# Optimization experiments

Hardware: AMD Instinct MI355X
Metric: run time of the kernel (lower is better)

The kernel has to match this reference:

```python
import jax, jax.numpy as jnp
import numpy as np

EMB = 8
HID = 64
B = 1000
T = 512
N = (B * T) // 5  # events per source; sources partition the (batch,time) grid

_KEYS = ["ccba", "cdtx", "cust", "dp", "remit"]
_NUMS = {"ccba": 8, "cdtx": 1, "cust": 1, "dp": 2, "remit": 1}
_CATS = {"ccba": 0, "cdtx": 2, "cust": 3, "dp": 8, "remit": 1}
_VOCAB = {"ccba": 0, "cdtx": 179, "cust": 37, "dp": 435, "remit": 5}


def setup_inputs() -> dict:
    ks = iter(jax.random.split(jax.random.key(0), 64))
    rng = np.random.default_rng(0)
    chunks = np.split(rng.permutation(B * T), 5)
    d = {}
    for k5, ch in zip(_KEYS, chunks):
        d[k5 + "_num"] = jax.random.normal(next(ks), (N, _NUMS[k5]), jnp.float32)
        if _CATS[k5] > 0:
            d[k5 + "_cat"] = jax.random.randint(next(ks), (N, _CATS[k5]), 0, _VOCAB[k5])
            d[k5 + "_tab"] = jax.random.normal(next(ks), (_VOCAB[k5], EMB), jnp.float32) * 0.1
        d[k5 + "_bi"] = jnp.asarray(ch // T, jnp.int32)
        d[k5 + "_ti"] = jnp.asarray(ch % T, jnp.int32)
        in_dim = _CATS[k5] * EMB + _NUMS[k5]
        d[k5 + "_W"] = jax.random.normal(next(ks), (in_dim, HID), jnp.float32) * np.float32(1.0 / np.sqrt(in_dim))
        d[k5 + "_b"] = jnp.zeros((HID,), jnp.float32)
    # LSTM: 2 layers x 2 directions, hidden 64, proj_size 1 -> layer1 input is 2
    for l, insz in [(0, HID), (1, 2)]:
        d[f"Wih{l}"] = jax.random.normal(next(ks), (2, 4 * HID, insz), jnp.float32) * 0.05
        d[f"Whh{l}"] = jax.random.normal(next(ks), (2, 4 * HID, 1), jnp.float32) * 0.05
        d[f"Whr{l}"] = jax.random.normal(next(ks), (2, 1, HID), jnp.float32) * 0.05
        d[f"bih{l}"] = jnp.zeros((2, 4 * HID), jnp.float32)
        d[f"bhh{l}"] = jnp.zeros((2, 4 * HID), jnp.float32)
    d["length"] = T
    d["batch_size"] = B
    return d


def _embed(num, cat, tab, W, b):
    # FeatureEmbedder: concat(categorical embeddings, numeric) -> Linear(hidden)
    x = num if cat is None else jnp.concatenate([tab[cat].reshape(cat.shape[0], -1), num], axis=-1)
    return x @ W + b


def _lstm_dir(x, Wih, Whh, Whr, bih, bhh, reverse):
    Bx = x.shape[0]
    H = Whr.shape[1]
    p = Whr.shape[0]
    bias = bih + bhh

    def step(carry, xt):
        h, c = carry  # h: [B,p] projected hidden, c: [B,H] cell
        g = xt @ Wih.T + h @ Whh.T + bias
        i, f, gg, o = jnp.split(g, 4, axis=-1)  # PyTorch gate order i,f,g,o
        c = jax.nn.sigmoid(f) * c + jax.nn.sigmoid(i) * jnp.tanh(gg)
        h = (jax.nn.sigmoid(o) * jnp.tanh(c)) @ Whr.T  # proj_size projection
        return (h, c), h

    init = (jnp.zeros((Bx, p), x.dtype), jnp.zeros((Bx, H), x.dtype))
    _, ys = jax.lax.scan(step, init, jnp.swapaxes(x, 0, 1), reverse=reverse)
    return jnp.swapaxes(ys, 0, 1)  # [B,T,p]


def _bilstm(x, Wih, Whh, Whr, bih, bhh):
    fwd = _lstm_dir(x, Wih[0], Whh[0], Whr[0], bih[0], bhh[0], False)
    bwd = _lstm_dir(x, Wih[1], Whh[1], Whr[1], bih[1], bhh[1], True)
    return jnp.concatenate([fwd, bwd], axis=-1)


def _forward(a):
    feat = jnp.zeros((a["batch_size"], a["length"], HID), jnp.float32)
    for k5 in _KEYS:
        v = _embed(a[k5 + "_num"], a.get(k5 + "_cat"), a.get(k5 + "_tab"), a[k5 + "_W"], a[k5 + "_b"])
        feat = feat.at[a[k5 + "_bi"], a[k5 + "_ti"]].set(v)  # scatter-assemble padded tensor
    h = _bilstm(feat, a["Wih0"], a["Whh0"], a["Whr0"], a["bih0"], a["bhh0"])
    h = _bilstm(h, a["Wih1"], a["Whh1"], a["Whr1"], a["bih1"], a["bhh1"])
    return h.mean(axis=2)  # [B,T]


def reference(ccba_num, ccba_bi, ccba_ti, ccba_W, ccba_b,
              cdtx_num, cdtx_cat, cdtx_tab, cdtx_bi, cdtx_ti, cdtx_W, cdtx_b,
              cust_num, cust_cat, cust_tab, cust_bi, cust_ti, cust_W, cust_b,
              dp_num, dp_cat, dp_tab, dp_bi, dp_ti, dp_W, dp_b,
              remit_num, remit_cat, remit_tab, remit_bi, remit_ti, remit_W, remit_b,
              Wih0, Whh0, Whr0, bih0, bhh0, Wih1, Whh1, Whr1, bih1, bhh1,
              length, batch_size):
    return _forward(dict(locals()))
```

## Files before the change

### kernel.cpp

```cpp
#include <hip/hip_runtime.h>
#include <cstdint>
#include <cstddef>

#define TLEN 512
#define BATCH 1000
#define NEV 102400
#define HID 64

__device__ __forceinline__ float fast_rcp(float x) {
#if __has_builtin(__builtin_amdgcn_rcpf)
    return __builtin_amdgcn_rcpf(x);
#else
    return 1.0f / x;
#endif
}
__device__ __forceinline__ float sigm(float x) { return fast_rcp(1.0f + __expf(-x)); }
__device__ __forceinline__ float tanh_f(float x) { return fmaf(2.0f, sigm(2.0f * x), -1.0f); }

__global__ __launch_bounds__(256) void embed_kernel(
    const float* __restrict__ num, const int* __restrict__ cat,
    const float* __restrict__ tab, const int* __restrict__ bi,
    const int* __restrict__ ti, const float* __restrict__ W,
    const float* __restrict__ bvec, float* __restrict__ feat,
    int n_num, int n_cat)
{
    int e = blockIdx.x * 4 + (threadIdx.x >> 6);
    int hh = threadIdx.x & 63;
    if (e >= NEV) return;
    float acc = bvec[hh];
    int j = 0;
    for (int c = 0; c < n_cat; ++c) {
        int idx = cat[e * n_cat + c];
        const float* trow = tab + (size_t)idx * 8;
#pragma unroll
        for (int u = 0; u < 8; ++u)
            acc = fmaf(trow[u], W[(j + u) * HID + hh], acc);
        j += 8;
    }
    for (int u = 0; u < n_num; ++u)
        acc = fmaf(num[(size_t)e * n_num + u], W[(j + u) * HID + hh], acc);
    int pos = bi[e] * TLEN + ti[e];
    feat[(size_t)pos * HID + hh] = acc;
}

__global__ __launch_bounds__(256, 2) void lstm0_kernel(
    const float* __restrict__ feat, const float* __restrict__ Wih,
    const float* __restrict__ Whh, const float* __restrict__ Whr,
    const float* __restrict__ bih, const float* __restrict__ bhh,
    float* __restrict__ h0)
{
    const int b0 = blockIdx.x * 4;
    const int dir = blockIdx.y;
    const int tid = threadIdx.x, lane = tid & 63, wv = tid >> 6;

    const float* wrow = Wih + (size_t)(dir * 256 + tid) * HID;
    float4 w[16];
#pragma unroll
    for (int i = 0; i < 16; ++i) w[i] = ((const float4*)wrow)[i];
    const float whh = Whh[dir * 256 + tid];
    const float bias = bih[dir * 256 + tid] + bhh[dir * 256 + tid];
    const float whr = Whr[dir * HID + lane];

    __shared__ float4 featb[2][4][16];
    __shared__ float gbuf[4][256];
    __shared__ __align__(16) float hbuf[4];

    float c = 0.0f;
    const float* fb = feat + (size_t)(b0 + wv) * TLEN * HID;
    float* h0b = h0 + ((size_t)(b0 + wv) * TLEN) * 2 + dir;

    const int t0 = dir ? (TLEN - 1) : 0;
    ((float*)featb[0][wv])[lane] = fb[(size_t)t0 * HID + lane];
    if (tid < 4) hbuf[tid] = 0.0f;
    __syncthreads();

    for (int t = 0; t < TLEN; ++t) {
        const int buf = t & 1;
        const int tt = dir ? (TLEN - 1 - t) : t;

        float nf = 0.0f;
        const int tn = dir ? (TLEN - 2 - t) : (t + 1);
        const bool pf = (t < TLEN - 1);
        if (pf) nf = fb[(size_t)tn * HID + lane];

        const float4 hp = *(const float4*)hbuf;

        float a0 = fmaf(whh, hp.x, bias);
        float a1 = fmaf(whh, hp.y, bias);
        float a2 = fmaf(whh, hp.z, bias);
        float a3 = fmaf(whh, hp.w, bias);
#pragma unroll
        for (int i = 0; i < 16; ++i) {
            float4 f0 = featb[buf][0][i];
            float4 f1 = featb[buf][1][i];
            float4 f2 = featb[buf][2][i];
            float4 f3 = featb[buf][3][i];
            a0 = fmaf(f0.x, w[i].x, a0); a0 = fmaf(f0.y, w[i].y, a0);
            a0 = fmaf(f0.z, w[i].z, a0); a0 = fmaf(f0.w, w[i].w, a0);
            a1 = fmaf(f1.x, w[i].x, a1); a1 = fmaf(f1.y, w[i].y, a1);
            a1 = fmaf(f1.z, w[i].z, a1); a1 = fmaf(f1.w, w[i].w, a1);
            a2 = fmaf(f2.x, w[i].x, a2); a2 = fmaf(f2.y, w[i].y, a2);
            a2 = fmaf(f2.z, w[i].z, a2); a2 = fmaf(f2.w, w[i].w, a2);
            a3 = fmaf(f3.x, w[i].x, a3); a3 = fmaf(f3.y, w[i].y, a3);
            a3 = fmaf(f3.z, w[i].z, a3); a3 = fmaf(f3.w, w[i].w, a3);
        }
        gbuf[0][tid] = a0;
        gbuf[1][tid] = a1;
        gbuf[2][tid] = a2;
        gbuf[3][tid] = a3;
        if (pf) ((float*)featb[1 - buf][wv])[lane] = nf;
        __syncthreads();

        const float gi = gbuf[wv][lane];
        const float gf = gbuf[wv][64 + lane];
        const float gg = gbuf[wv][128 + lane];
        const float go = gbuf[wv][192 + lane];
        c = sigm(gf) * c + sigm(gi) * tanh_f(gg);
        float p = sigm(go) * tanh_f(c) * whr;
#pragma unroll
        for (int off = 1; off < 64; off <<= 1) p += __shfl_xor(p, off, 64);
        if (lane == 0) {
            hbuf[wv] = p;
            h0b[(size_t)tt * 2] = p;
        }
        __syncthreads();
    }
}

__global__ __launch_bounds__(256) void lstm1_kernel(
    const float* __restrict__ h0, const float* __restrict__ Wih,
    const float* __restrict__ Whh, const float* __restrict__ Whr,
    const float* __restrict__ bih, const float* __restrict__ bhh,
    float* __restrict__ h1)
{
    int w = threadIdx.x >> 6, lane = threadIdx.x & 63;
    int p = blockIdx.x * 4 + w;
    int b = p >> 1, dir = p & 1;

    float wi0[4], wi1[4], whh[4], bias[4];
#pragma unroll
    for (int k = 0; k < 4; ++k) {
        int r = k * 64 + lane;
        wi0[k] = Wih[(size_t)(dir * 256 + r) * 2 + 0];
        wi1[k] = Wih[(size_t)(dir * 256 + r) * 2 + 1];
        whh[k] = Whh[dir * 256 + r];
        bias[k] = bih[dir * 256 + r] + bhh[dir * 256 + r];
    }
    float whr = Whr[dir * HID + lane];
    float h = 0.0f, c = 0.0f;
    const float* hb = h0 + (size_t)b * TLEN * 2;

    for (int t = 0; t < TLEN; ++t) {
        int tt = dir ? (TLEN - 1 - t) : t;
        float x0 = hb[tt * 2], x1 = hb[tt * 2 + 1];
        float g[4];
#pragma unroll
        for (int k = 0; k < 4; ++k)
            g[k] = fmaf(whh[k], h, fmaf(wi1[k], x1, fmaf(wi0[k], x0, bias[k])));
        c = sigm(g[1]) * c + sigm(g[0]) * tanh_f(g[2]);
        float pp = sigm(g[3]) * tanh_f(c) * whr;
#pragma unroll
        for (int off = 1; off < 64; off <<= 1) pp += __shfl_xor(pp, off, 64);
        h = pp;
        if (lane == 0) h1[((size_t)b * TLEN + tt) * 2 + dir] = h;
    }
}

__global__ __launch_bounds__(256) void mean_kernel(
    const float2* __restrict__ h1, float* __restrict__ out)
{
    int i = blockIdx.x * 256 + threadIdx.x;
    if (i < BATCH * TLEN) {
        float2 v = h1[i];
        out[i] = 0.5f * (v.x + v.y);
    }
}

extern "C" void kernel_launch(void* const* d_in, const int* in_sizes, int n_in,
                              void* d_out, int out_size, void* d_ws, size_t ws_size,
                              hipStream_t stream)
{
    const float* ccba_num = (const float*)d_in[0];
    const int*   ccba_bi  = (const int*)d_in[1];
    const int*   ccba_ti  = (const int*)d_in[2];
    const float* ccba_W   = (const float*)d_in[3];
    const float* ccba_b   = (const float*)d_in[4];
    const float* cdtx_num = (const float*)d_in[5];
    const int*   cdtx_cat = (const int*)d_in[6];
    const float* cdtx_tab = (const float*)d_in[7];
    const int*   cdtx_bi  = (const int*)d_in[8];
    const int*   cdtx_ti  = (const int*)d_in[9];
    const float* cdtx_W   = (const float*)d_in[10];
    const float* cdtx_b   = (const float*)d_in[11];
    const float* cust_num = (const float*)d_in[12];
    const int*   cust_cat = (const int*)d_in[13];
    const float* cust_tab = (const float*)d_in[14];
    const int*   cust_bi  = (const int*)d_in[15];
    const int*   cust_ti  = (const int*)d_in[16];
    const float* cust_W   = (const float*)d_in[17];
    const float* cust_b   = (const float*)d_in[18];
    const float* dp_num   = (const float*)d_in[19];
    const int*   dp_cat   = (const int*)d_in[20];
    const float* dp_tab   = (const float*)d_in[21];
    const int*   dp_bi    = (const int*)d_in[22];
    const int*   dp_ti    = (const int*)d_in[23];
    const float* dp_W     = (const float*)d_in[24];
    const float* dp_b     = (const float*)d_in[25];
    const float* remit_num = (const float*)d_in[26];
    const int*   remit_cat = (const int*)d_in[27];
    const float* remit_tab = (const float*)d_in[28];
    const int*   remit_bi  = (const int*)d_in[29];
    const int*   remit_ti  = (const int*)d_in[30];
    const float* remit_W   = (const float*)d_in[31];
    const float* remit_b   = (const float*)d_in[32];
    const float* Wih0 = (const float*)d_in[33];
    const float* Whh0 = (const float*)d_in[34];
    const float* Whr0 = (const float*)d_in[35];
    const float* bih0 = (const float*)d_in[36];
    const float* bhh0 = (const float*)d_in[37];
    const float* Wih1 = (const float*)d_in[38];
    const float* Whh1 = (const float*)d_in[39];
    const float* Whr1 = (const float*)d_in[40];
    const float* bih1 = (const float*)d_in[41];
    const float* bhh1 = (const float*)d_in[42];

    char* ws = (char*)d_ws;
    float* feat = (float*)ws;
    float* h0   = (float*)(ws + 131072000);
    float* h1   = (float*)(ws + 135168000);
    float* out  = (float*)d_out;

    dim3 blk(256);
    int eg = (NEV + 3) / 4;

    embed_kernel<<<eg, blk, 0, stream>>>(ccba_num, nullptr, nullptr, ccba_bi, ccba_ti, ccba_W, ccba_b, feat, 8, 0);
    embed_kernel<<<eg, blk, 0, stream>>>(cdtx_num, cdtx_cat, cdtx_tab, cdtx_bi, cdtx_ti, cdtx_W, cdtx_b, feat, 1, 2);
    embed_kernel<<<eg, blk, 0, stream>>>(cust_num, cust_cat, cust_tab, cust_bi, cust_ti, cust_W, cust_b, feat, 1, 3);
    embed_kernel<<<eg, blk, 0, stream>>>(dp_num, dp_cat, dp_tab, dp_bi, dp_ti, dp_W, dp_b, feat, 2, 8);
    embed_kernel<<<eg, blk, 0, stream>>>(remit_num, remit_cat, remit_tab, remit_bi, remit_ti, remit_W, remit_b, feat, 1, 1);

    lstm0_kernel<<<dim3(BATCH / 4, 2), blk, 0, stream>>>(feat, Wih0, Whh0, Whr0, bih0, bhh0, h0);
    lstm1_kernel<<<(BATCH * 2) / 4, blk, 0, stream>>>(h0, Wih1, Whh1, Whr1, bih1, bhh1, h1);
    mean_kernel<<<(BATCH * TLEN + 255) / 256, blk, 0, stream>>>((const float2*)h1, out);
}
```

Before: 1.567 ms.

## Fold embedding Linear into LSTM input projection and precompute gate preactivations

Composes each source's embedding weight and bias with layer-0 Wih (plus the LSTM biases) into small per-source matrices. Each event is then projected straight to 512 gate preactivations, scattered into a gate buffer, so the recurrent kernel only adds Whh*h with no per-step matvec or block syncs. The recurrent loops are also unrolled by two with register prefetch of the next steps. This trades the per-step 64x256 matvec for about 1 GB of gate-buffer writes and reads, and only runs if the workspace is large enough, otherwise the old path is kept.

```diff
diff --git a/kernel.cpp b/kernel.cpp
--- a/kernel.cpp
+++ b/kernel.cpp
@@ -16,6 +16,205 @@
 }
 __device__ __forceinline__ float sigm(float x) { return fast_rcp(1.0f + __expf(-x)); }
 __device__ __forceinline__ float tanh_f(float x) { return fmaf(2.0f, sigm(2.0f * x), -1.0f); }
+
+
+__global__ __launch_bounds__(512) void compose_kernel(
+    const float* __restrict__ W0, const float* __restrict__ B0,
+    const float* __restrict__ W1, const float* __restrict__ B1,
+    const float* __restrict__ W2, const float* __restrict__ B2,
+    const float* __restrict__ W3, const float* __restrict__ B3,
+    const float* __restrict__ W4, const float* __restrict__ B4,
+    const float* __restrict__ Wih, const float* __restrict__ bih,
+    const float* __restrict__ bhh, float* __restrict__ wp)
+{
+    const int col = threadIdx.x;
+    const int row = blockIdx.x;
+    const float* srcW; const float* srcB; int base, IND;
+    if (row < 9)        { srcW = W0; srcB = B0; base = 0;   IND = 8;  }
+    else if (row < 27)  { srcW = W1; srcB = B1; base = 9;   IND = 17; }
+    else if (row < 53)  { srcW = W2; srcB = B2; base = 27;  IND = 25; }
+    else if (row < 120) { srcW = W3; srcB = B3; base = 53;  IND = 66; }
+    else                { srcW = W4; srcB = B4; base = 120; IND = 9;  }
+    const int j = row - base;
+    const float* xrow = (j < IND) ? (srcW + (size_t)j * 64) : srcB;
+    const float* wr = Wih + (size_t)col * 64;
+    float acc = 0.0f;
+#pragma unroll
+    for (int h2 = 0; h2 < 64; ++h2) acc = fmaf(xrow[h2], wr[h2], acc);
+    if (j == IND) acc += bih[col] + bhh[col];
+    wp[(size_t)row * 512 + col] = acc;
+}
+
+template<int NNUM, int NCAT>
+__global__ __launch_bounds__(512) void project_kernel(
+    const float* __restrict__ num, const int* __restrict__ cat,
+    const float* __restrict__ tab, const int* __restrict__ bi,
+    const int* __restrict__ ti, const float* __restrict__ wp,
+    float* __restrict__ gpre)
+{
+    constexpr int IND = NCAT * 8 + NNUM;
+    const int col = threadIdx.x;
+    float wcol[IND];
+#pragma unroll
+    for (int j = 0; j < IND; ++j) wcol[j] = wp[(size_t)j * 512 + col];
+    const float bcol = wp[(size_t)IND * 512 + col];
+
+    for (int ev = blockIdx.x; ev < NEV; ev += gridDim.x) {
+        const int pos = bi[ev] * TLEN + ti[ev];
+        float acc = bcol;
+#pragma unroll
+        for (int c0 = 0; c0 < NCAT; ++c0) {
+            const int idx = cat[ev * NCAT + c0];
+            const float* tr = tab + (size_t)idx * 8;
+#pragma unroll
+            for (int u = 0; u < 8; ++u)
+                acc = fmaf(tr[u], wcol[c0 * 8 + u], acc);
+        }
+#pragma unroll
+        for (int u = 0; u < NNUM; ++u)
+            acc = fmaf(num[(size_t)ev * NNUM + u], wcol[NCAT * 8 + u], acc);
+        gpre[(size_t)pos * 512 + col] = acc;
+    }
+}
+
+__global__ __launch_bounds__(256) void rec0_kernel(
+    const float* __restrict__ gpre, const float* __restrict__ Whh,
+    const float* __restrict__ Whr, float* __restrict__ h0)
+{
+    const int wv = threadIdx.x >> 6, lane = threadIdx.x & 63;
+    const int p = blockIdx.x * 4 + wv;
+    const int b = p >> 1, dir = p & 1;
+
+    float whh4[4];
+#pragma unroll
+    for (int k = 0; k < 4; ++k) whh4[k] = Whh[dir * 256 + k * 64 + lane];
+    const float whr = Whr[dir * HID + lane];
+
+    const float* gb = gpre + (size_t)dir * 256 + lane;
+    float* h0p = h0 + (size_t)b * TLEN * 2 + dir;
+
+    auto addr = [&](int t) -> const float* {
+        int tc = t < TLEN ? t : TLEN - 1;
+        int tt = dir ? (TLEN - 1 - tc) : tc;
+        return gb + ((size_t)(b * TLEN + tt)) * 512;
+    };
+
+    float A[4], B[4];
+    {
+        const float* pa = addr(0); const float* pb = addr(1);
+#pragma unroll
+        for (int k = 0; k < 4; ++k) { A[k] = pa[k * 64]; B[k] = pb[k * 64]; }
+    }
+    float h = 0.0f, c = 0.0f;
+
+    for (int t = 0; t < TLEN; t += 2) {
+        float C[4], D[4];
+        const float* pc = addr(t + 2); const float* pd = addr(t + 3);
+#pragma unroll
+        for (int k = 0; k < 4; ++k) { C[k] = pc[k * 64]; D[k] = pd[k * 64]; }
+
+        {
+            float gi = fmaf(whh4[0], h, A[0]);
+            float gf = fmaf(whh4[1], h, A[1]);
+            float gg = fmaf(whh4[2], h, A[2]);
+            float go = fmaf(whh4[3], h, A[3]);
+            c = sigm(gf) * c + sigm(gi) * tanh_f(gg);
+            float pp = sigm(go) * tanh_f(c) * whr;
+#pragma unroll
+            for (int off = 1; off < 64; off <<= 1) pp += __shfl_xor(pp, off, 64);
+            h = pp;
+            int tt = dir ? (TLEN - 1 - t) : t;
+            if (lane == 0) h0p[(size_t)tt * 2] = h;
+        }
+        {
+            float gi = fmaf(whh4[0], h, B[0]);
+            float gf = fmaf(whh4[1], h, B[1]);
+            float gg = fmaf(whh4[2], h, B[2]);
+            float go = fmaf(whh4[3], h, B[3]);
+            c = sigm(gf) * c + sigm(gi) * tanh_f(gg);
+            float pp = sigm(go) * tanh_f(c) * whr;
+#pragma unroll
+            for (int off = 1; off < 64; off <<= 1) pp += __shfl_xor(pp, off, 64);
+            h = pp;
+            int tt = dir ? (TLEN - 2 - t) : (t + 1);
+            if (lane == 0) h0p[(size_t)tt * 2] = h;
+        }
+#pragma unroll
+        for (int k = 0; k < 4; ++k) { A[k] = C[k]; B[k] = D[k]; }
+    }
+}
+
+__global__ __launch_bounds__(256) void lstm1_kernel(
+    const float* __restrict__ h0, const float* __restrict__ Wih,
+    const float* __restrict__ Whh, const float* __restrict__ Whr,
+    const float* __restrict__ bih, const float* __restrict__ bhh,
+    float* __restrict__ h1)
+{
+    int w = threadIdx.x >> 6, lane = threadIdx.x & 63;
+    int p = blockIdx.x * 4 + w;
+    int b = p >> 1, dir = p & 1;
+
+    float wi0[4], wi1[4], whh[4], bias[4];
+#pragma unroll
+    for (int k = 0; k < 4; ++k) {
+        int r = k * 64 + lane;
+        wi0[k] = Wih[(size_t)(dir * 256 + r) * 2 + 0];
+        wi1[k] = Wih[(size_t)(dir * 256 + r) * 2 + 1];
+        whh[k] = Whh[dir * 256 + r];
+        bias[k] = bih[dir * 256 + r] + bhh[dir * 256 + r];
+    }
+    float whr = Whr[dir * HID + lane];
+    float h = 0.0f, c = 0.0f;
+    const float* hb = h0 + (size_t)b * TLEN * 2;
+
+    auto xat = [&](int t) -> float2 {
+        int tc = t < TLEN ? t : TLEN - 1;
+        int tt = dir ? (TLEN - 1 - tc) : tc;
+        return *(const float2*)(hb + (size_t)tt * 2);
+    };
+
+    float2 xA = xat(0), xB = xat(1);
+    for (int t = 0; t < TLEN; t += 2) {
+        float2 xC = xat(t + 2), xD = xat(t + 3);
+        {
+            float g[4];
+#pragma unroll
+            for (int k = 0; k < 4; ++k)
+                g[k] = fmaf(whh[k], h, fmaf(wi1[k], xA.y, fmaf(wi0[k], xA.x, bias[k])));
+            c = sigm(g[1]) * c + sigm(g[0]) * tanh_f(g[2]);
+            float pp = sigm(g[3]) * tanh_f(c) * whr;
+#pragma unroll
+            for (int off = 1; off < 64; off <<= 1) pp += __shfl_xor(pp, off, 64);
+            h = pp;
+            int tt = dir ? (TLEN - 1 - t) : t;
+            if (lane == 0) h1[((size_t)b * TLEN + tt) * 2 + dir] = h;
+        }
+        {
+            float g[4];
+#pragma unroll
+            for (int k = 0; k < 4; ++k)
+                g[k] = fmaf(whh[k], h, fmaf(wi1[k], xB.y, fmaf(wi0[k], xB.x, bias[k])));
+            c = sigm(g[1]) * c + sigm(g[0]) * tanh_f(g[2]);
+            float pp = sigm(g[3]) * tanh_f(c) * whr;
+#pragma unroll
+            for (int off = 1; off < 64; off <<= 1) pp += __shfl_xor(pp, off, 64);
+            h = pp;
+            int tt = dir ? (TLEN - 2 - t) : (t + 1);
+            if (lane == 0) h1[((size_t)b * TLEN + tt) * 2 + dir] = h;
+        }
+        xA = xC; xB = xD;
+    }
+}
+
+__global__ __launch_bounds__(256) void mean_kernel(
+    const float2* __restrict__ h1, float* __restrict__ out)
+{
+    int i = blockIdx.x * 256 + threadIdx.x;
+    if (i < BATCH * TLEN) {
+        float2 v = h1[i];
+        out[i] = 0.5f * (v.x + v.y);
+    }
+}
 
 __global__ __launch_bounds__(256) void embed_kernel(
     const float* __restrict__ num, const int* __restrict__ cat,
@@ -77,14 +276,11 @@
     for (int t = 0; t < TLEN; ++t) {
         const int buf = t & 1;
         const int tt = dir ? (TLEN - 1 - t) : t;
-
         float nf = 0.0f;
         const int tn = dir ? (TLEN - 2 - t) : (t + 1);
         const bool pf = (t < TLEN - 1);
         if (pf) nf = fb[(size_t)tn * HID + lane];
-
         const float4 hp = *(const float4*)hbuf;
-
         float a0 = fmaf(whh, hp.x, bias);
         float a1 = fmaf(whh, hp.y, bias);
         float a2 = fmaf(whh, hp.z, bias);
@@ -110,7 +306,6 @@
         gbuf[3][tid] = a3;
         if (pf) ((float*)featb[1 - buf][wv])[lane] = nf;
         __syncthreads();
-
         const float gi = gbuf[wv][lane];
         const float gf = gbuf[wv][64 + lane];
         const float gg = gbuf[wv][128 + lane];
@@ -124,55 +319,6 @@
             h0b[(size_t)tt * 2] = p;
         }
         __syncthreads();
-    }
-}
-
-__global__ __launch_bounds__(256) void lstm1_kernel(
-    const float* __restrict__ h0, const float* __restrict__ Wih,
-    const float* __restrict__ Whh, const float* __restrict__ Whr,
-    const float* __restrict__ bih, const float* __restrict__ bhh,
-    float* __restrict__ h1)
-{
-    int w = threadIdx.x >> 6, lane = threadIdx.x & 63;
-    int p = blockIdx.x * 4 + w;
-    int b = p >> 1, dir = p & 1;
-
-    float wi0[4], wi1[4], whh[4], bias[4];
-#pragma unroll
-    for (int k = 0; k < 4; ++k) {
-        int r = k * 64 + lane;
-        wi0[k] = Wih[(size_t)(dir * 256 + r) * 2 + 0];
-        wi1[k] = Wih[(size_t)(dir * 256 + r) * 2 + 1];
-        whh[k] = Whh[dir * 256 + r];
-        bias[k] = bih[dir * 256 + r] + bhh[dir * 256 + r];
-    }
-    float whr = Whr[dir * HID + lane];
-    float h = 0.0f, c = 0.0f;
-    const float* hb = h0 + (size_t)b * TLEN * 2;
-
-    for (int t = 0; t < TLEN; ++t) {
-        int tt = dir ? (TLEN - 1 - t) : t;
-        float x0 = hb[tt * 2], x1 = hb[tt * 2 + 1];
-        float g[4];
-#pragma unroll
-        for (int k = 0; k < 4; ++k)
-            g[k] = fmaf(whh[k], h, fmaf(wi1[k], x1, fmaf(wi0[k], x0, bias[k])));
-        c = sigm(g[1]) * c + sigm(g[0]) * tanh_f(g[2]);
-        float pp = sigm(g[3]) * tanh_f(c) * whr;
-#pragma unroll
-        for (int off = 1; off < 64; off <<= 1) pp += __shfl_xor(pp, off, 64);
-        h = pp;
-        if (lane == 0) h1[((size_t)b * TLEN + tt) * 2 + dir] = h;
-    }
-}
-
-__global__ __launch_bounds__(256) void mean_kernel(
-    const float2* __restrict__ h1, float* __restrict__ out)
-{
-    int i = blockIdx.x * 256 + threadIdx.x;
-    if (i < BATCH * TLEN) {
-        float2 v = h1[i];
-        out[i] = 0.5f * (v.x + v.y);
     }
 }
 
@@ -224,22 +370,48 @@
     const float* bih1 = (const float*)d_in[41];
     const float* bhh1 = (const float*)d_in[42];
 
-    char* ws = (char*)d_ws;
-    float* feat = (float*)ws;
-    float* h0   = (float*)(ws + 131072000);
-    float* h1   = (float*)(ws + 135168000);
-    float* out  = (float*)d_out;
-
+    float* out = (float*)d_out;
     dim3 blk(256);
-    int eg = (NEV + 3) / 4;
-
-    embed_kernel<<<eg, blk, 0, stream>>>(ccba_num, nullptr, nullptr, ccba_bi, ccba_ti, ccba_W, ccba_b, feat, 8, 0);
-    embed_kernel<<<eg, blk, 0, stream>>>(cdtx_num, cdtx_cat, cdtx_tab, cdtx_bi, cdtx_ti, cdtx_W, cdtx_b, feat, 1, 2);
-    embed_kernel<<<eg, blk, 0, stream>>>(cust_num, cust_cat, cust_tab, cust_bi, cust_ti, cust_W, cust_b, feat, 1, 3);
-    embed_kernel<<<eg, blk, 0, stream>>>(dp_num, dp_cat, dp_tab, dp_bi, dp_ti, dp_W, dp_b, feat, 2, 8);
-    embed_kernel<<<eg, blk, 0, stream>>>(remit_num, remit_cat, remit_tab, remit_bi, remit_ti, remit_W, remit_b, feat, 1, 1);
-
-    lstm0_kernel<<<dim3(BATCH / 4, 2), blk, 0, stream>>>(feat, Wih0, Whh0, Whr0, bih0, bhh0, h0);
-    lstm1_kernel<<<(BATCH * 2) / 4, blk, 0, stream>>>(h0, Wih1, Whh1, Whr1, bih1, bhh1, h1);
-    mean_kernel<<<(BATCH * TLEN + 255) / 256, blk, 0, stream>>>((const float2*)h1, out);
-}
+
+    const size_t GPRE_BYTES = (size_t)512000 * 512 * 4;
+    const size_t H0_OFF = GPRE_BYTES;
+    const size_t H1_OFF = H0_OFF + 4096000;
+    const size_t WP_OFF = H1_OFF + 4096000;
+    const size_t NEED   = WP_OFF + 130 * 512 * 4;
+
+    if (ws_size >= NEED) {
+        char* ws = (char*)d_ws;
+        float* gpre = (float*)ws;
+        float* h0   = (float*)(ws + H0_OFF);
+        float* h1   = (float*)(ws + H1_OFF);
+        float* wp   = (float*)(ws + WP_OFF);
+
+        compose_kernel<<<130, 512, 0, stream>>>(
+            ccba_W, ccba_b, cdtx_W, cdtx_b, cust_W, cust_b,
+            dp_W, dp_b, remit_W, remit_b, Wih0, bih0, bhh0, wp);
+
+        project_kernel<8, 0><<<512, 512, 0, stream>>>(ccba_num, nullptr, nullptr, ccba_bi, ccba_ti, wp + (size_t)0 * 512, gpre);
+        project_kernel<1, 2><<<512, 512, 0, stream>>>(cdtx_num, cdtx_cat, cdtx_tab, cdtx_bi, cdtx_ti, wp + (size_t)9 * 512, gpre);
+        project_kernel<1, 3><<<512, 512, 0, stream>>>(cust_num, cust_cat, cust_tab, cust_bi, cust_ti, wp + (size_t)27 * 512, gpre);
+        project_kernel<2, 8><<<512, 512, 0, stream>>>(dp_num, dp_cat, dp_tab, dp_bi, dp_ti, wp + (size_t)53 * 512, gpre);
+        project_kernel<1, 1><<<512, 512, 0, stream>>>(remit_num, remit_cat, remit_tab, remit_bi, remit_ti, wp + (size_t)120 * 512, gpre);
+
+        rec0_kernel<<<500, blk, 0, stream>>>(gpre, Whh0, Whr0, h0);
+        lstm1_kernel<<<500, blk, 0, stream>>>(h0, Wih1, Whh1, Whr1, bih1, bhh1, h1);
+        mean_kernel<<<(BATCH * TLEN + 255) / 256, blk, 0, stream>>>((const float2*)h1, out);
+    } else {
+        char* ws = (char*)d_ws;
+        float* feat = (float*)ws;
+        float* h0   = (float*)(ws + 131072000);
+        float* h1   = (float*)(ws + 135168000);
+        int eg = (NEV + 3) / 4;
+        embed_kernel<<<eg, blk, 0, stream>>>(ccba_num, nullptr, nullptr, ccba_bi, ccba_ti, ccba_W, ccba_b, feat, 8, 0);
+        embed_kernel<<<eg, blk, 0, stream>>>(cdtx_num, cdtx_cat, cdtx_tab, cdtx_bi, cdtx_ti, cdtx_W, cdtx_b, feat, 1, 2);
+        embed_kernel<<<eg, blk, 0, stream>>>(cust_num, cust_cat, cust_tab, cust_bi, cust_ti, cust_W, cust_b, feat, 1, 3);
+        embed_kernel<<<eg, blk, 0, stream>>>(dp_num, dp_cat, dp_tab, dp_bi, dp_ti, dp_W, dp_b, feat, 2, 8);
+        embed_kernel<<<eg, blk, 0, stream>>>(remit_num, remit_cat, remit_tab, remit_bi, remit_ti, remit_W, remit_b, feat, 1, 1);
+        lstm0_kernel<<<dim3(BATCH / 4, 2), blk, 0, stream>>>(feat, Wih0, Whh0, Whr0, bih0, bhh0, h0);
+        lstm1_kernel<<<500, blk, 0, stream>>>(h0, Wih1, Whh1, Whr1, bih1, bhh1, h1);
+        mean_kernel<<<(BATCH * TLEN + 255) / 256, blk, 0, stream>>>((const float2*)h1, out);
+    }
+}
```

New measurement: 1.562 ms. Within noise of the previous version (-0.3%).
